# Kernel tuning notes

Measured on AMD Instinct MI355X. Metric: run time of the kernel, lower is better.

## Reference

```python
import jax, jax.numpy as jnp
import numpy as np

N_NODES = 50000
N_EDGES = 1250000
IN_CH = 64
HID = 64
N_CLASSES = 10
N_GRAPHS = 128


def _xavier(key, shape):
    fan_out, fan_in = shape
    limit = np.sqrt(6.0 / (fan_in + fan_out))
    return jax.random.uniform(key, shape, jnp.float32, -limit, limit)


def setup_inputs() -> dict:
    key = jax.random.key(0)
    ks = jax.random.split(key, 12)
    x = jax.random.normal(ks[0], (N_NODES, IN_CH), jnp.float32)
    edge_index = jax.random.randint(ks[1], (2, N_EDGES), 0, N_NODES, jnp.int64)
    batch = jnp.sort(jax.random.randint(ks[2], (N_NODES,), 0, N_GRAPHS, jnp.int64))
    return {
        "x": x,
        "edge_index": edge_index,
        "batch": batch,
        # GraphConv i: lin_rel (weight+bias) applied to aggregated neighbors,
        # lin_root (no bias) applied to self features. Weights are [out, in].
        "W1_rel": _xavier(ks[3], (HID, IN_CH)), "b1": jnp.zeros((HID,), jnp.float32),
        "W1_root": _xavier(ks[4], (HID, IN_CH)),
        "W2_rel": _xavier(ks[5], (HID, HID)), "b2": jnp.zeros((HID,), jnp.float32),
        "W2_root": _xavier(ks[6], (HID, HID)),
        "W3_rel": _xavier(ks[7], (HID, HID)), "b3": jnp.zeros((HID,), jnp.float32),
        "W3_root": _xavier(ks[8], (HID, HID)),
        "W_lin": _xavier(ks[9], (N_CLASSES, HID)), "b_lin": jnp.zeros((N_CLASSES,), jnp.float32),
    }


def _graph_conv(x, src, dst, W_rel, b, W_root):
    # sum-aggregate neighbor features: gather at src, scatter-add at dst
    agg = jax.ops.segment_sum(x[src], dst, num_segments=N_NODES)  # [N, F]
    return agg @ W_rel.T + b + x @ W_root.T


def reference(x, edge_index, batch, W1_rel, b1, W1_root, W2_rel, b2, W2_root,
              W3_rel, b3, W3_root, W_lin, b_lin):
    src, dst = edge_index[0], edge_index[1]
    h = jax.nn.relu(_graph_conv(x, src, dst, W1_rel, b1, W1_root))
    h = jax.nn.relu(_graph_conv(h, src, dst, W2_rel, b2, W2_root))
    h = _graph_conv(h, src, dst, W3_rel, b3, W3_root)
    # global mean pool over graphs
    sums = jax.ops.segment_sum(h, batch, num_segments=N_GRAPHS)        # [G, HID]
    counts = jax.ops.segment_sum(jnp.ones((h.shape[0],), h.dtype), batch,
                                 num_segments=N_GRAPHS)
    pooled = sums / jnp.maximum(counts, 1.0)[:, None]
    out = pooled @ W_lin.T + b_lin  # dropout inactive in eval mode
    return (pooled, out)
```

## Files before the change

kernel.cpp:

```cpp
#include <hip/hip_runtime.h>

#define N_NODES   50000
#define HID       64
#define N_GRAPHS  128
#define N_CLASSES 10
#define NP        196
#define EPA       8192
#define PCAP      8192

typedef __attribute__((ext_vector_type(8))) short short8;
typedef __attribute__((ext_vector_type(4))) float f32x4;

__device__ __forceinline__ unsigned bf16rne(float f) {
    unsigned u = __float_as_uint(f);
    return (u + 0x7fffu + ((u >> 16) & 1u)) >> 16;
}
__device__ __forceinline__ unsigned pack_bf16x2(float lo, float hi) {
    return bf16rne(lo) | (bf16rne(hi) << 16);
}



__global__ void cvt_kernel(const float* __restrict__ x, unsigned short* __restrict__ xb,
                           int* __restrict__ gcursor, const int* __restrict__ batch,
                           int* __restrict__ gstart) {
    int i = blockIdx.x * blockDim.x + threadIdx.x;
    if (blockIdx.x == 0 && threadIdx.x < NP) gcursor[threadIdx.x] = 0;
    if (i < N_NODES) {
        int b = batch[i];
        int bp = (i > 0) ? batch[i - 1] : -1;
        for (int g = bp + 1; g <= b; ++g) gstart[g] = i;
        if (i == N_NODES - 1)
            for (int g = b + 1; g <= N_GRAPHS; ++g) gstart[g] = N_NODES;
    }
    if (i < N_NODES * 16) {
        float4 v = ((const float4*)x)[i];
        uint2 o;
        o.x = pack_bf16x2(v.x, v.y);
        o.y = pack_bf16x2(v.z, v.w);
        ((uint2*)xb)[i] = o;
    }
}


__global__ __launch_bounds__(256) void bucket_kernel(
    const int* __restrict__ src, const int* __restrict__ dst,
    int* __restrict__ gcursor, unsigned* __restrict__ packed, int E) {
    __shared__ int hist[NP], scp[NP], base[NP], cnt2[NP];
    __shared__ int sc[256];
    __shared__ unsigned stag[EPA];
    const int t = threadIdx.x;
    const int e0 = blockIdx.x * EPA;
    const int e1 = min(e0 + EPA, E);
    for (int i = t; i < NP; i += 256) { hist[i] = 0; cnt2[i] = 0; }
    __syncthreads();
    for (int e = e0 + t; e < e1; e += 256)
        atomicAdd(&hist[dst[e] >> 8], 1);
    __syncthreads();
    sc[t] = (t < NP) ? hist[t] : 0;
    __syncthreads();
    for (int off = 1; off < 256; off <<= 1) {
        int add = (t >= off) ? sc[t - off] : 0;
        __syncthreads();
        sc[t] += add;
        __syncthreads();
    }
    if (t < NP) {
        scp[t] = sc[t] - hist[t];
        if (hist[t] > 0) base[t] = atomicAdd(&gcursor[t], hist[t]);
    }
    __syncthreads();
    for (int e = e0 + t; e < e1; e += 256) {
        int d = dst[e], s = src[e];
        int p = d >> 8;
        int idx = scp[p] + atomicAdd(&cnt2[p], 1);
        stag[idx] = (unsigned)s | ((unsigned)(d & 255) << 16) | ((unsigned)p << 24);
    }
    __syncthreads();
    const int n = e1 - e0;
    for (int i = t; i < n; i += 256) {
        unsigned v = stag[i];
        int p = v >> 24;
        packed[(size_t)p * PCAP + base[p] + (i - scp[p])] = v & 0x00FFFFFFu;
    }
}

__global__ __launch_bounds__(256) void build_kernel(
    const unsigned* __restrict__ packed, const int* __restrict__ gcursor,
    int* __restrict__ offsets, unsigned short* __restrict__ csr,
    int* __restrict__ sums_zero) {
    __shared__ int hist[256], lofs[256], cnt[256], sc[256], gv[256];
    __shared__ unsigned short lcsr[PCAP];
    const int p = blockIdx.x, t = threadIdx.x;

    if (p == 0) {
        for (int i = t; i < N_GRAPHS * 64; i += 256) sums_zero[i] = 0;
    }

    int v = (t < NP) ? gcursor[t] : 0;
    sc[t] = v; gv[t] = v;
    __syncthreads();
    for (int off = 1; off < 256; off <<= 1) {
        int add = (t >= off) ? sc[t - off] : 0;
        __syncthreads();
        sc[t] += add;
        __syncthreads();
    }
    const int pb = sc[p] - gv[p];
    const int ne = gv[p];
    if (p == NP - 1 && t == 0) offsets[N_NODES] = sc[NP - 1];
    __syncthreads();

    const unsigned* mypk = packed + (size_t)p * PCAP;
    hist[t] = 0; cnt[t] = 0;
    __syncthreads();
    for (int i = t; i < ne; i += 256)
        atomicAdd(&hist[(mypk[i] >> 16) & 255], 1);
    __syncthreads();
    sc[t] = hist[t];
    __syncthreads();
    for (int off = 1; off < 256; off <<= 1) {
        int add = (t >= off) ? sc[t - off] : 0;
        __syncthreads();
        sc[t] += add;
        __syncthreads();
    }
    lofs[t] = sc[t] - hist[t];
    int node = p * 256 + t;
    if (node < N_NODES) offsets[node] = pb + lofs[t];
    __syncthreads();
    for (int i = t; i < ne; i += 256) {
        unsigned vv = mypk[i];
        int dl = (vv >> 16) & 255;
        int slot = lofs[dl] + atomicAdd(&cnt[dl], 1);
        lcsr[slot] = (unsigned short)(vv & 0xFFFFu);
    }
    __syncthreads();
    for (int i = t; i < ne; i += 256) csr[pb + i] = lcsr[i];
}


template <int RELU, int POOL>
__global__ __launch_bounds__(256) void layer_kernel(
    const unsigned short* __restrict__ hin,
    const int* __restrict__ offsets, const unsigned short* __restrict__ csr_src,
    const float* __restrict__ Wrel, const float* __restrict__ bias,
    const float* __restrict__ Wroot, unsigned short* __restrict__ hout,
    const int* __restrict__ batch, float* __restrict__ sums) {
    __shared__ short8 wfrag[2][4][2][4][16];
    __shared__ unsigned short agg_lds[64][72];

    const int tid = threadIdx.x;
    const int w = tid >> 6, lane = tid & 63;
    const int g0 = (blockIdx.x * 4 + w) * 16;

    for (int f = tid; f < 1024; f += 256) {
        int m = f >> 9;
        int r = f & 511;
        int t = r >> 7, s = (r >> 6) & 1, q = (r >> 4) & 3, c = r & 15;
        const float* W = m ? Wroot : Wrel;
        const float4* pw = (const float4*)(W + (t * 16 + c) * 64 + s * 32 + q * 8);
        float4 v0 = pw[0], v1 = pw[1];
        short8 fr;
        fr[0] = (short)bf16rne(v0.x); fr[1] = (short)bf16rne(v0.y);
        fr[2] = (short)bf16rne(v0.z); fr[3] = (short)bf16rne(v0.w);
        fr[4] = (short)bf16rne(v1.x); fr[5] = (short)bf16rne(v1.y);
        fr[6] = (short)bf16rne(v1.z); fr[7] = (short)bf16rne(v1.w);
        wfrag[m][t][s][q][c] = fr;
    }

    if (g0 < N_NODES) {
        const int rg = lane >> 3;
        const int cg = lane & 7;
        int myoff = (lane < 17) ? offsets[g0 + lane] : 0;
        for (int i = 0; i < 16; ++i) {
            const int beg = __shfl(myoff, i), end = __shfl(myoff, i + 1);
            float acc[8] = {0.f, 0.f, 0.f, 0.f, 0.f, 0.f, 0.f, 0.f};
            for (int base = beg; base < end; base += 64) {
                int cnt = min(64, end - base);
                int sidx = (base + lane < end) ? (int)csr_src[base + lane] : 0;
                for (int kb = 0; kb < cnt; kb += 32) {
                    uint4 u[4];
#pragma unroll
                    for (int p = 0; p < 4; ++p) {
                        int e = kb + 8 * p + rg;
                        int r = __shfl(sidx, e);
                        u[p] = (e < cnt) ? *((const uint4*)(hin + (size_t)r * 64) + cg)
                                         : make_uint4(0u, 0u, 0u, 0u);
                    }
#pragma unroll
                    for (int p = 0; p < 4; ++p) {
                        acc[0] += __uint_as_float(u[p].x << 16);
                        acc[1] += __uint_as_float(u[p].x & 0xffff0000u);
                        acc[2] += __uint_as_float(u[p].y << 16);
                        acc[3] += __uint_as_float(u[p].y & 0xffff0000u);
                        acc[4] += __uint_as_float(u[p].z << 16);
                        acc[5] += __uint_as_float(u[p].z & 0xffff0000u);
                        acc[6] += __uint_as_float(u[p].w << 16);
                        acc[7] += __uint_as_float(u[p].w & 0xffff0000u);
                    }
                }
            }
#pragma unroll
            for (int m = 8; m <= 32; m <<= 1)
#pragma unroll
                for (int j = 0; j < 8; ++j)
                    acc[j] += __shfl_xor(acc[j], m);
            if (rg == 0) {
                uint4 o;
                o.x = pack_bf16x2(acc[0], acc[1]);
                o.y = pack_bf16x2(acc[2], acc[3]);
                o.z = pack_bf16x2(acc[4], acc[5]);
                o.w = pack_bf16x2(acc[6], acc[7]);
                *((uint4*)&agg_lds[w * 16 + i][cg * 8]) = o;
            }
        }
    }

    __syncthreads();
    if (g0 >= N_NODES) return;

    const int q = lane >> 4, c = lane & 15;
    short8 a_agg[2], a_x[2];
#pragma unroll
    for (int s = 0; s < 2; ++s) {
        a_agg[s] = *(const short8*)&agg_lds[w * 16 + c][s * 32 + q * 8];
        a_x[s]   = *(const short8*)(hin + (size_t)(g0 + c) * 64 + s * 32 + q * 8);
    }
    float biasv[4];
#pragma unroll
    for (int t = 0; t < 4; ++t) biasv[t] = bias[t * 16 + c];

    f32x4 acc4[4];
#pragma unroll
    for (int t = 0; t < 4; ++t) {
        f32x4 a0 = {biasv[t], biasv[t], biasv[t], biasv[t]};
        a0 = __builtin_amdgcn_mfma_f32_16x16x32_bf16(a_agg[0], wfrag[0][t][0][q][c], a0, 0, 0, 0);
        a0 = __builtin_amdgcn_mfma_f32_16x16x32_bf16(a_agg[1], wfrag[0][t][1][q][c], a0, 0, 0, 0);
        a0 = __builtin_amdgcn_mfma_f32_16x16x32_bf16(a_x[0],   wfrag[1][t][0][q][c], a0, 0, 0, 0);
        a0 = __builtin_amdgcn_mfma_f32_16x16x32_bf16(a_x[1],   wfrag[1][t][1][q][c], a0, 0, 0, 0);
        acc4[t] = a0;
    }

    if (POOL) {
        int b0 = batch[g0], b15 = batch[g0 + 15];
        if (b0 == b15) {
#pragma unroll
            for (int t = 0; t < 4; ++t) {
                float s = acc4[t][0] + acc4[t][1] + acc4[t][2] + acc4[t][3];
                s += __shfl_xor(s, 16);
                s += __shfl_xor(s, 32);
                if (q == 0) atomicAdd(&sums[b0 * 64 + t * 16 + c], s);
            }
        } else {
#pragma unroll
            for (int r = 0; r < 4; ++r) {
                int bq = batch[g0 + q * 4 + r];
#pragma unroll
                for (int t = 0; t < 4; ++t)
                    atomicAdd(&sums[bq * 64 + t * 16 + c], acc4[t][r]);
            }
        }
    } else {
#pragma unroll
        for (int t = 0; t < 4; ++t)
#pragma unroll
            for (int r = 0; r < 4; ++r) {
                float v = acc4[t][r];
                if (RELU) v = fmaxf(v, 0.f);
                agg_lds[w * 16 + q * 4 + r][t * 16 + c] = (unsigned short)bf16rne(v);
            }
#pragma unroll
        for (int it = 0; it < 2; ++it) {
            int row = it * 8 + (lane >> 3);
            int ch = (lane & 7) * 8;
            short8 v = *(const short8*)&agg_lds[w * 16 + row][ch];
            *(short8*)(hout + (size_t)(g0 + row) * 64 + ch) = v;
        }
    }
}


__global__ void final_kernel(const float* __restrict__ sums, const int* __restrict__ gstart,
                             const float* __restrict__ Wlin, const float* __restrict__ blin,
                             float* __restrict__ out) {
    __shared__ float pl[64];
    int g = blockIdx.x, lane = threadIdx.x;
    float cdiv = fmaxf((float)(gstart[g + 1] - gstart[g]), 1.0f);
    float p = sums[g * 64 + lane] / cdiv;
    out[g * 64 + lane] = p;
    pl[lane] = p;
    __syncthreads();
    if (lane < N_CLASSES) {
        float o = blin[lane];
#pragma unroll
        for (int k = 0; k < 64; ++k) o += pl[k] * Wlin[lane * 64 + k];
        out[N_GRAPHS * 64 + g * N_CLASSES + lane] = o;
    }
}


extern "C" void kernel_launch(void* const* d_in, const int* in_sizes, int n_in,
                              void* d_out, int out_size, void* d_ws, size_t ws_size,
                              hipStream_t stream) {
    const float* x     = (const float*)d_in[0];
    const int*   ei    = (const int*)d_in[1];
    const int*   batch = (const int*)d_in[2];
    const float* W1r = (const float*)d_in[3];
    const float* b1  = (const float*)d_in[4];
    const float* W1o = (const float*)d_in[5];
    const float* W2r = (const float*)d_in[6];
    const float* b2  = (const float*)d_in[7];
    const float* W2o = (const float*)d_in[8];
    const float* W3r = (const float*)d_in[9];
    const float* b3  = (const float*)d_in[10];
    const float* W3o = (const float*)d_in[11];
    const float* Wl  = (const float*)d_in[12];
    const float* bl  = (const float*)d_in[13];
    float* out = (float*)d_out;

    const int E = in_sizes[1] / 2;
    const int* src = ei;
    const int* dst = ei + E;

    char* p = (char*)d_ws;
    unsigned short* xb  = (unsigned short*)p; p += (size_t)N_NODES * 64 * 2;
    unsigned short* h1  = (unsigned short*)p; p += (size_t)N_NODES * 64 * 2;
    unsigned short* h2  = (unsigned short*)p; p += (size_t)N_NODES * 64 * 2;
    unsigned* packed    = (unsigned*)p; p += (size_t)NP * PCAP * 4;
    unsigned short* csr = (unsigned short*)p; p += (size_t)E * 2;
    int* offsets   = (int*)p;   p += (size_t)(N_NODES + 1) * 4;
    int* gcursor   = (int*)p;   p += NP * 4;
    float* sums    = (float*)p; p += (size_t)N_GRAPHS * 64 * 4;
    int* gstart    = (int*)p;   p += (N_GRAPHS + 1) * 4;

    const int NCHUNK = (E + EPA - 1) / EPA;
    cvt_kernel<<<(N_NODES * 16 + 255) / 256, 256, 0, stream>>>(x, xb, gcursor, batch, gstart);
    bucket_kernel<<<NCHUNK, 256, 0, stream>>>(src, dst, gcursor, packed, E);
    build_kernel<<<NP, 256, 0, stream>>>(packed, gcursor, offsets, csr, (int*)sums);

    const int LB = (N_NODES + 63) / 64;
    layer_kernel<1, 0><<<LB, 256, 0, stream>>>(xb, offsets, csr, W1r, b1, W1o, h1, batch, sums);
    layer_kernel<1, 0><<<LB, 256, 0, stream>>>(h1, offsets, csr, W2r, b2, W2o, h2, batch, sums);
    layer_kernel<0, 1><<<LB, 256, 0, stream>>>(h2, offsets, csr, W3r, b3, W3o, h1, batch, sums);

    final_kernel<<<N_GRAPHS, 64, 0, stream>>>(sums, gstart, Wl, bl, out);
}
```

Before: 250.8 us.

## Halve nodes per block and split MFMA output tiles across wave pairs

Each layer block now covers 32 nodes instead of 64, each wave aggregating 8 nodes. In the MFMA phase, pairs of waves share one 16-node tile and each computes half of the output columns. This doubles the block count to improve load balance and shorten the serial aggregation per wave. In exchange, every block reloads and converts the weight fragments again, and extra barriers and bounds checks are added.

New measurement: 234.2 us (median of 3 runs). -6.6%, faster.

```diff
diff --git a/kernel.cpp b/kernel.cpp
--- a/kernel.cpp
+++ b/kernel.cpp
@@ -148,11 +148,11 @@
     const float* __restrict__ Wroot, unsigned short* __restrict__ hout,
     const int* __restrict__ batch, float* __restrict__ sums) {
     __shared__ short8 wfrag[2][4][2][4][16];
-    __shared__ unsigned short agg_lds[64][72];
+    __shared__ unsigned short agg_lds[32][72];
 
     const int tid = threadIdx.x;
     const int w = tid >> 6, lane = tid & 63;
-    const int g0 = (blockIdx.x * 4 + w) * 16;
+    const int g0 = blockIdx.x * 32;
 
     for (int f = tid; f < 1024; f += 256) {
         int m = f >> 9;
@@ -169,11 +169,12 @@
         wfrag[m][t][s][q][c] = fr;
     }
 
-    if (g0 < N_NODES) {
+    {
         const int rg = lane >> 3;
         const int cg = lane & 7;
-        int myoff = (lane < 17) ? offsets[g0 + lane] : 0;
-        for (int i = 0; i < 16; ++i) {
+        const int nb = g0 + w * 8;
+        int myoff = (lane < 9) ? offsets[min(nb + lane, N_NODES)] : 0;
+        for (int i = 0; i < 8; ++i) {
             const int beg = __shfl(myoff, i), end = __shfl(myoff, i + 1);
             float acc[8] = {0.f, 0.f, 0.f, 0.f, 0.f, 0.f, 0.f, 0.f};
             for (int base = beg; base < end; base += 64) {
@@ -212,42 +213,47 @@
                 o.y = pack_bf16x2(acc[2], acc[3]);
                 o.z = pack_bf16x2(acc[4], acc[5]);
                 o.w = pack_bf16x2(acc[6], acc[7]);
-                *((uint4*)&agg_lds[w * 16 + i][cg * 8]) = o;
+                *((uint4*)&agg_lds[w * 8 + i][cg * 8]) = o;
             }
         }
     }
 
     __syncthreads();
-    if (g0 >= N_NODES) return;
-
+
+    const int ng = w >> 1;
+    const int th = w & 1;
     const int q = lane >> 4, c = lane & 15;
+    const int n0 = g0 + ng * 16;
+
     short8 a_agg[2], a_x[2];
 #pragma unroll
     for (int s = 0; s < 2; ++s) {
-        a_agg[s] = *(const short8*)&agg_lds[w * 16 + c][s * 32 + q * 8];
-        a_x[s]   = *(const short8*)(hin + (size_t)(g0 + c) * 64 + s * 32 + q * 8);
-    }
-    float biasv[4];
-#pragma unroll
-    for (int t = 0; t < 4; ++t) biasv[t] = bias[t * 16 + c];
-
-    f32x4 acc4[4];
-#pragma unroll
-    for (int t = 0; t < 4; ++t) {
-        f32x4 a0 = {biasv[t], biasv[t], biasv[t], biasv[t]};
+        a_agg[s] = *(const short8*)&agg_lds[ng * 16 + c][s * 32 + q * 8];
+        a_x[s]   = *(const short8*)(hin + (size_t)min(n0 + c, N_NODES - 1) * 64 + s * 32 + q * 8);
+    }
+
+    f32x4 acc4[2];
+#pragma unroll
+    for (int tt = 0; tt < 2; ++tt) {
+        const int t = th * 2 + tt;
+        float bv = bias[t * 16 + c];
+        f32x4 a0 = {bv, bv, bv, bv};
         a0 = __builtin_amdgcn_mfma_f32_16x16x32_bf16(a_agg[0], wfrag[0][t][0][q][c], a0, 0, 0, 0);
         a0 = __builtin_amdgcn_mfma_f32_16x16x32_bf16(a_agg[1], wfrag[0][t][1][q][c], a0, 0, 0, 0);
         a0 = __builtin_amdgcn_mfma_f32_16x16x32_bf16(a_x[0],   wfrag[1][t][0][q][c], a0, 0, 0, 0);
         a0 = __builtin_amdgcn_mfma_f32_16x16x32_bf16(a_x[1],   wfrag[1][t][1][q][c], a0, 0, 0, 0);
-        acc4[t] = a0;
+        acc4[tt] = a0;
     }
 
     if (POOL) {
-        int b0 = batch[g0], b15 = batch[g0 + 15];
+        int nlast = n0 + 15;
+        int b0 = batch[min(n0, N_NODES - 1)];
+        int b15 = (nlast < N_NODES) ? batch[nlast] : -1;
         if (b0 == b15) {
 #pragma unroll
-            for (int t = 0; t < 4; ++t) {
-                float s = acc4[t][0] + acc4[t][1] + acc4[t][2] + acc4[t][3];
+            for (int tt = 0; tt < 2; ++tt) {
+                const int t = th * 2 + tt;
+                float s = acc4[tt][0] + acc4[tt][1] + acc4[tt][2] + acc4[tt][3];
                 s += __shfl_xor(s, 16);
                 s += __shfl_xor(s, 32);
                 if (q == 0) atomicAdd(&sums[b0 * 64 + t * 16 + c], s);
@@ -255,27 +261,36 @@
         } else {
 #pragma unroll
             for (int r = 0; r < 4; ++r) {
-                int bq = batch[g0 + q * 4 + r];
-#pragma unroll
-                for (int t = 0; t < 4; ++t)
-                    atomicAdd(&sums[bq * 64 + t * 16 + c], acc4[t][r]);
+                int n = n0 + q * 4 + r;
+                if (n < N_NODES) {
+                    int bq = batch[n];
+#pragma unroll
+                    for (int tt = 0; tt < 2; ++tt)
+                        atomicAdd(&sums[bq * 64 + (th * 2 + tt) * 16 + c], acc4[tt][r]);
+                }
             }
         }
     } else {
-#pragma unroll
-        for (int t = 0; t < 4; ++t)
+        __syncthreads();
+#pragma unroll
+        for (int tt = 0; tt < 2; ++tt) {
+            const int t = th * 2 + tt;
 #pragma unroll
             for (int r = 0; r < 4; ++r) {
-                float v = acc4[t][r];
+                float v = acc4[tt][r];
                 if (RELU) v = fmaxf(v, 0.f);
-                agg_lds[w * 16 + q * 4 + r][t * 16 + c] = (unsigned short)bf16rne(v);
-            }
-#pragma unroll
-        for (int it = 0; it < 2; ++it) {
-            int row = it * 8 + (lane >> 3);
+                agg_lds[ng * 16 + q * 4 + r][t * 16 + c] = (unsigned short)bf16rne(v);
+            }
+        }
+        __syncthreads();
+        {
+            int row = w * 8 + (lane >> 3);
             int ch = (lane & 7) * 8;
-            short8 v = *(const short8*)&agg_lds[w * 16 + row][ch];
-            *(short8*)(hout + (size_t)(g0 + row) * 64 + ch) = v;
+            int n = g0 + row;
+            if (n < N_NODES) {
+                short8 v = *(const short8*)&agg_lds[row][ch];
+                *(short8*)(hout + (size_t)n * 64 + ch) = v;
+            }
         }
     }
 }
@@ -339,7 +354,7 @@
     bucket_kernel<<<NCHUNK, 256, 0, stream>>>(src, dst, gcursor, packed, E);
     build_kernel<<<NP, 256, 0, stream>>>(packed, gcursor, offsets, csr, (int*)sums);
 
-    const int LB = (N_NODES + 63) / 64;
+    const int LB = (N_NODES + 31) / 32;
     layer_kernel<1, 0><<<LB, 256, 0, stream>>>(xb, offsets, csr, W1r, b1, W1o, h1, batch, sums);
     layer_kernel<1, 0><<<LB, 256, 0, stream>>>(h1, offsets, csr, W2r, b2, W2o, h2, batch, sums);
     layer_kernel<0, 1><<<LB, 256, 0, stream>>>(h2, offsets, csr, W3r, b3, W3o, h1, batch, sums);
```

## Shrink layer blocks to 16 nodes, split MFMA output tiles across waves

Applied to the files above, without the earlier changes.

Each layer block now covers 16 nodes instead of 64. Each wave aggregates 4 nodes, then computes one 16-column output tile with MFMA instead of all four. This gives about four times as many blocks and shrinks LDS per block, which should improve load balance across CUs and occupancy, helped by a launch bound of 8 blocks. The cost is redoing the weight-fragment conversion in four times as many blocks, plus extra block-wide barriers. Separately, the edge chunk size for bucketing is halved, which doubles the number of bucket blocks.

After: 237.2 us. 5.4% less time.

```diff
diff --git a/kernel.cpp b/kernel.cpp
--- a/kernel.cpp
+++ b/kernel.cpp
@@ -5,7 +5,7 @@
 #define N_GRAPHS  128
 #define N_CLASSES 10
 #define NP        196
-#define EPA       8192
+#define EPA       4096
 #define PCAP      8192
 
 typedef __attribute__((ext_vector_type(8))) short short8;
@@ -141,18 +141,18 @@
 
 
 template <int RELU, int POOL>
-__global__ __launch_bounds__(256) void layer_kernel(
+__global__ __launch_bounds__(256, 8) void layer_kernel(
     const unsigned short* __restrict__ hin,
     const int* __restrict__ offsets, const unsigned short* __restrict__ csr_src,
     const float* __restrict__ Wrel, const float* __restrict__ bias,
     const float* __restrict__ Wroot, unsigned short* __restrict__ hout,
     const int* __restrict__ batch, float* __restrict__ sums) {
     __shared__ short8 wfrag[2][4][2][4][16];
-    __shared__ unsigned short agg_lds[64][72];
+    __shared__ unsigned short agg_lds[16][72];
 
     const int tid = threadIdx.x;
     const int w = tid >> 6, lane = tid & 63;
-    const int g0 = (blockIdx.x * 4 + w) * 16;
+    const int g0 = blockIdx.x * 16;
 
     for (int f = tid; f < 1024; f += 256) {
         int m = f >> 9;
@@ -169,11 +169,12 @@
         wfrag[m][t][s][q][c] = fr;
     }
 
-    if (g0 < N_NODES) {
+    {
         const int rg = lane >> 3;
         const int cg = lane & 7;
-        int myoff = (lane < 17) ? offsets[g0 + lane] : 0;
-        for (int i = 0; i < 16; ++i) {
+        const int nb = g0 + w * 4;
+        int myoff = (lane < 5) ? offsets[nb + lane] : 0;
+        for (int i = 0; i < 4; ++i) {
             const int beg = __shfl(myoff, i), end = __shfl(myoff, i + 1);
             float acc[8] = {0.f, 0.f, 0.f, 0.f, 0.f, 0.f, 0.f, 0.f};
             for (int base = beg; base < end; base += 64) {
@@ -212,69 +213,57 @@
                 o.y = pack_bf16x2(acc[2], acc[3]);
                 o.z = pack_bf16x2(acc[4], acc[5]);
                 o.w = pack_bf16x2(acc[6], acc[7]);
-                *((uint4*)&agg_lds[w * 16 + i][cg * 8]) = o;
+                *((uint4*)&agg_lds[w * 4 + i][cg * 8]) = o;
             }
         }
     }
 
     __syncthreads();
-    if (g0 >= N_NODES) return;
 
     const int q = lane >> 4, c = lane & 15;
+    const int t = w;
+
     short8 a_agg[2], a_x[2];
 #pragma unroll
     for (int s = 0; s < 2; ++s) {
-        a_agg[s] = *(const short8*)&agg_lds[w * 16 + c][s * 32 + q * 8];
+        a_agg[s] = *(const short8*)&agg_lds[c][s * 32 + q * 8];
         a_x[s]   = *(const short8*)(hin + (size_t)(g0 + c) * 64 + s * 32 + q * 8);
     }
-    float biasv[4];
-#pragma unroll
-    for (int t = 0; t < 4; ++t) biasv[t] = bias[t * 16 + c];
-
-    f32x4 acc4[4];
-#pragma unroll
-    for (int t = 0; t < 4; ++t) {
-        f32x4 a0 = {biasv[t], biasv[t], biasv[t], biasv[t]};
-        a0 = __builtin_amdgcn_mfma_f32_16x16x32_bf16(a_agg[0], wfrag[0][t][0][q][c], a0, 0, 0, 0);
-        a0 = __builtin_amdgcn_mfma_f32_16x16x32_bf16(a_agg[1], wfrag[0][t][1][q][c], a0, 0, 0, 0);
-        a0 = __builtin_amdgcn_mfma_f32_16x16x32_bf16(a_x[0],   wfrag[1][t][0][q][c], a0, 0, 0, 0);
-        a0 = __builtin_amdgcn_mfma_f32_16x16x32_bf16(a_x[1],   wfrag[1][t][1][q][c], a0, 0, 0, 0);
-        acc4[t] = a0;
-    }
+
+    float bv = bias[t * 16 + c];
+    f32x4 a0 = {bv, bv, bv, bv};
+    a0 = __builtin_amdgcn_mfma_f32_16x16x32_bf16(a_agg[0], wfrag[0][t][0][q][c], a0, 0, 0, 0);
+    a0 = __builtin_amdgcn_mfma_f32_16x16x32_bf16(a_agg[1], wfrag[0][t][1][q][c], a0, 0, 0, 0);
+    a0 = __builtin_amdgcn_mfma_f32_16x16x32_bf16(a_x[0],   wfrag[1][t][0][q][c], a0, 0, 0, 0);
+    a0 = __builtin_amdgcn_mfma_f32_16x16x32_bf16(a_x[1],   wfrag[1][t][1][q][c], a0, 0, 0, 0);
 
     if (POOL) {
         int b0 = batch[g0], b15 = batch[g0 + 15];
         if (b0 == b15) {
-#pragma unroll
-            for (int t = 0; t < 4; ++t) {
-                float s = acc4[t][0] + acc4[t][1] + acc4[t][2] + acc4[t][3];
-                s += __shfl_xor(s, 16);
-                s += __shfl_xor(s, 32);
-                if (q == 0) atomicAdd(&sums[b0 * 64 + t * 16 + c], s);
-            }
+            float s = a0[0] + a0[1] + a0[2] + a0[3];
+            s += __shfl_xor(s, 16);
+            s += __shfl_xor(s, 32);
+            if (q == 0) atomicAdd(&sums[b0 * 64 + t * 16 + c], s);
         } else {
 #pragma unroll
             for (int r = 0; r < 4; ++r) {
                 int bq = batch[g0 + q * 4 + r];
-#pragma unroll
-                for (int t = 0; t < 4; ++t)
-                    atomicAdd(&sums[bq * 64 + t * 16 + c], acc4[t][r]);
+                atomicAdd(&sums[bq * 64 + t * 16 + c], a0[r]);
             }
         }
     } else {
-#pragma unroll
-        for (int t = 0; t < 4; ++t)
-#pragma unroll
-            for (int r = 0; r < 4; ++r) {
-                float v = acc4[t][r];
-                if (RELU) v = fmaxf(v, 0.f);
-                agg_lds[w * 16 + q * 4 + r][t * 16 + c] = (unsigned short)bf16rne(v);
-            }
-#pragma unroll
-        for (int it = 0; it < 2; ++it) {
-            int row = it * 8 + (lane >> 3);
-            int ch = (lane & 7) * 8;
-            short8 v = *(const short8*)&agg_lds[w * 16 + row][ch];
+        __syncthreads();
+#pragma unroll
+        for (int r = 0; r < 4; ++r) {
+            float v = a0[r];
+            if (RELU) v = fmaxf(v, 0.f);
+            agg_lds[q * 4 + r][t * 16 + c] = (unsigned short)bf16rne(v);
+        }
+        __syncthreads();
+        if (tid < 128) {
+            int row = tid >> 3;
+            int ch = (tid & 7) * 8;
+            short8 v = *(const short8*)&agg_lds[row][ch];
             *(short8*)(hout + (size_t)(g0 + row) * 64 + ch) = v;
         }
     }
@@ -339,7 +328,7 @@
     bucket_kernel<<<NCHUNK, 256, 0, stream>>>(src, dst, gcursor, packed, E);
     build_kernel<<<NP, 256, 0, stream>>>(packed, gcursor, offsets, csr, (int*)sums);
 
-    const int LB = (N_NODES + 63) / 64;
+    const int LB = N_NODES / 16;
     layer_kernel<1, 0><<<LB, 256, 0, stream>>>(xb, offsets, csr, W1r, b1, W1o, h1, batch, sums);
     layer_kernel<1, 0><<<LB, 256, 0, stream>>>(h1, offsets, csr, W2r, b2, W2o, h2, batch, sums);
     layer_kernel<0, 1><<<LB, 256, 0, stream>>>(h2, offsets, csr, W3r, b3, W3o, h1, batch, sums);
```
